# Optimization experiments

Measured on AMD Instinct MI355X. Metric: run time of the kernel, lower is better.

Reference implementation:

```python
import jax, jax.numpy as jnp
import numpy as np
from jax import lax

B, T, N = 4, 48, 2000
F, H, HEADS, HOR, K = 16, 64, 4, 24, 3
P = H // 2
EPS_BN = 1e-5
EPS_LN = 1e-5
NEG = -1e9


def layer_norm(x, g, b):
    mu = jnp.mean(x, axis=-1, keepdims=True)
    var = jnp.var(x, axis=-1, keepdims=True)
    return (x - mu) * jax.lax.rsqrt(var + EPS_LN) * g + b


def setup_inputs() -> dict:
    key = jax.random.key(0)
    ks = jax.random.split(key, 16)
    s = lambda k, shp, sc: jax.random.normal(k, shp, jnp.float32) * sc
    return {
        "x": s(ks[0], (B, T, N), 1.0),
        "conv_w": s(ks[1], (F, 1, K), 0.3),
        "conv_b": jnp.zeros((F,), jnp.float32),
        "bn_g": jnp.ones((F,), jnp.float32),
        "bn_b": jnp.zeros((F,), jnp.float32),
        "proj_w": s(ks[2], (H, F * T), 0.03),
        "proj_b": jnp.zeros((H,), jnp.float32),
        "ln1_g": jnp.ones((H,), jnp.float32),
        "ln1_b": jnp.zeros((H,), jnp.float32),
        "src_w": s(ks[3], (P, H), 0.1),
        "src_b": jnp.zeros((P,), jnp.float32),
        "dst_w": s(ks[4], (P, H), 0.1),
        "dst_b": jnp.zeros((P,), jnp.float32),
        "edge_scale": jnp.ones((1,), jnp.float32),
        "in_proj_w": s(ks[5], (3 * H, H), 0.1),
        "in_proj_b": jnp.zeros((3 * H,), jnp.float32),
        "out_w": s(ks[6], (H, H), 0.1),
        "out_b": jnp.zeros((H,), jnp.float32),
        "lnA_g": jnp.ones((H,), jnp.float32),
        "lnA_b": jnp.zeros((H,), jnp.float32),
        "pred_w": s(ks[7], (HOR, H), 0.1),
        "pred_b": jnp.zeros((HOR,), jnp.float32),
    }


def reference(x, conv_w, conv_b, bn_g, bn_b, proj_w, proj_b, ln1_g, ln1_b,
              src_w, src_b, dst_w, dst_b, edge_scale,
              in_proj_w, in_proj_b, out_w, out_b, lnA_g, lnA_b,
              pred_w, pred_b):
    # ---- temporal encoding: [B,T,N] -> [B*N,1,T] conv1d(same) ----
    xt = jnp.transpose(x, (0, 2, 1)).reshape(B * N, 1, T)
    h = lax.conv_general_dilated(xt, conv_w, (1,), "SAME",
                                 dimension_numbers=("NCH", "OIH", "NCH"))
    h = h + conv_b[None, :, None]
    # BatchNorm1d in eval mode (running_mean=0, running_var=1)
    h = h * (bn_g * lax.rsqrt(jnp.float32(1.0 + EPS_BN)))[None, :, None] + bn_b[None, :, None]
    h = jax.nn.relu(h)
    # ---- feature projector: flatten [F,T] -> hidden ----
    flat = h.reshape(B * N, F * T)
    z = flat @ proj_w.T + proj_b
    z = jax.nn.relu(layer_norm(z, ln1_g, ln1_b))
    node = z.reshape(B, N, H)
    # ---- dynamic graph generation ----
    src = jax.nn.leaky_relu(node @ src_w.T + src_b, 0.2)  # [B,N,P]
    dst = jax.nn.leaky_relu(node @ dst_w.T + dst_b, 0.2)
    adj = jnp.einsum("bnp,bmp->bnm", src, dst) * edge_scale[0]
    norm = jnp.maximum(jnp.linalg.norm(adj, axis=-1, keepdims=True), 1e-12)
    adj = adj / norm + jnp.eye(N, dtype=adj.dtype)[None]
    neg_mask = jnp.where(adj <= 0, jnp.float32(NEG), jnp.float32(0.0))  # [B,N,N]
    # ---- relational attention (single layer) ----
    residual = node
    qkv = node @ in_proj_w.T + in_proj_b  # [B,N,3H]
    q, k, v = jnp.split(qkv, 3, axis=-1)
    d = H // HEADS
    qh = q.reshape(B, N, HEADS, d)
    kh = k.reshape(B, N, HEADS, d)
    vh = v.reshape(B, N, HEADS, d)
    scores = jnp.einsum("bqhd,bkhd->bhqk", qh, kh) / jnp.sqrt(jnp.float32(d))
    attn = jax.nn.softmax(scores, axis=-1)
    y = jnp.einsum("bhqk,bkhd->bqhd", attn, vh).reshape(B, N, H)
    y = y @ out_w.T + out_b
    # second (adjacency-masked) attention recompute
    w2 = jnp.einsum("bnd,bmd->bnm", y, y) / jnp.sqrt(jnp.float32(H)) + neg_mask
    w2 = jax.nn.softmax(w2, axis=-1)
    y = jnp.einsum("bnm,bmd->bnd", w2, y)
    y = layer_norm(y + residual, lnA_g, lnA_b)
    # ---- horizon predictor ----
    return y @ pred_w.T + pred_b  # [B,N,HOR]
```

## Files before the change

kernel.cpp:

```cpp
#include <hip/hip_runtime.h>
#include <hip/hip_bf16.h>


#define NB 4
#define TT 48
#define NNODES 2000
#define HORZ 24

#define D4(a,b) ((a).x*(b).x + (a).y*(b).y + (a).z*(b).z + (a).w*(b).w)
#define FMA4(o,p,v) { (o).x = fmaf((p),(v).x,(o).x); (o).y = fmaf((p),(v).y,(o).y); \
                      (o).z = fmaf((p),(v).z,(o).z); (o).w = fmaf((p),(v).w,(o).w); }

__device__ __forceinline__ float wsum64(float v) {
#pragma unroll
    for (int m = 1; m < 64; m <<= 1) v += __shfl_xor(v, m, 64);
    return v;
}

__global__ __launch_bounds__(256) void k_tr(const float* __restrict__ pw,
                                            float* __restrict__ pT) {
    int i = blockIdx.x * 256 + threadIdx.x;
    int h = i / 768, j = i - h * 768;
    pT[((j >> 2) * 64 + h) * 4 + (j & 3)] = pw[i];
}

__global__ __launch_bounds__(64) void k_enc(const float* __restrict__ x,
        const float* __restrict__ cw, const float* __restrict__ cb,
        const float* __restrict__ bg, const float* __restrict__ bb,
        const float* __restrict__ pT, const float* __restrict__ pb,
        const float* __restrict__ g1, const float* __restrict__ b1,
        float* __restrict__ node) {
    __shared__ float xs[8][52];
    __shared__ float hs[8][768];
    __shared__ float wc[16][4];
    int tid = threadIdx.x;
    int g0 = blockIdx.x * 8;

    if (tid < 16) {
        float s = bg[tid] * rsqrtf(1.0f + 1e-5f);
        wc[tid][0] = cw[tid * 3 + 0] * s;
        wc[tid][1] = cw[tid * 3 + 1] * s;
        wc[tid][2] = cw[tid * 3 + 2] * s;
        wc[tid][3] = cb[tid] * s + bb[tid];
    }
    for (int i = tid; i < 8 * TT; i += 64) {
        int m = i & 7, t = i >> 3;
        int g = g0 + m;
        int b = g / NNODES, n = g - b * NNODES;
        xs[m][t + 1] = x[(b * TT + t) * NNODES + n];
    }
    if (tid < 8) { xs[tid][0] = 0.f; xs[tid][TT + 1] = 0.f; }
    __syncthreads();

    for (int m = 0; m < 8; m++) {
        for (int j = tid; j < 16 * TT; j += 64) {
            int f = j / TT, t = j - f * TT;
            float h = wc[f][0] * xs[m][t] + wc[f][1] * xs[m][t + 1] +
                      wc[f][2] * xs[m][t + 2] + wc[f][3];
            hs[m][j] = fmaxf(h, 0.f);
        }
    }
    __syncthreads();

    float acc[8];
    float pbv = pb[tid];
#pragma unroll
    for (int m = 0; m < 8; m++) acc[m] = pbv;
    const float4* pT4v = (const float4*)pT;
    for (int jb = 0; jb < 192; ++jb) {
        float4 wv = pT4v[jb * 64 + tid];
#pragma unroll
        for (int m = 0; m < 8; m++) {
            float4 hv = *(const float4*)&hs[m][jb * 4];
            acc[m] += D4(wv, hv);
        }
    }
    float gg = g1[tid], bbv = b1[tid];
    for (int m = 0; m < 8; m++) {
        float v = acc[m];
        float sm = wsum64(v);
        float sq = wsum64(v * v);
        float mu = sm * (1.f / 64.f);
        float var = sq * (1.f / 64.f) - mu * mu;
        float z = (v - mu) * rsqrtf(var + 1e-5f) * gg + bbv;
        node[(g0 + m) * 64 + tid] = fmaxf(z, 0.f);
    }
}

__global__ __launch_bounds__(256) void k_qkv(const float* __restrict__ node,
        const float* __restrict__ ipw, const float* __restrict__ ipb,
        const float* __restrict__ sw, const float* __restrict__ sb,
        const float* __restrict__ dw, const float* __restrict__ db,
        float* __restrict__ Qb, float* __restrict__ Kb, float* __restrict__ Vb,
        float* __restrict__ Sb, float* __restrict__ Db) {
    __shared__ float nds[8][64];
    int tid = threadIdx.x;
    int g0 = blockIdx.x * 8;
    for (int i = tid; i < 8 * 64; i += 256) {
        nds[i >> 6][i & 63] = node[(size_t)g0 * 64 + i];
    }
    __syncthreads();

    int o = tid;
    const float* wrow; float bias;
    if (o < 192)      { wrow = ipw + o * 64;          bias = ipb[o]; }
    else if (o < 224) { wrow = sw + (o - 192) * 64;   bias = sb[o - 192]; }
    else              { wrow = dw + (o - 224) * 64;   bias = db[o - 224]; }

    float acc[8];
#pragma unroll
    for (int n = 0; n < 8; ++n) acc[n] = bias;

#pragma unroll
    for (int c = 0; c < 4; ++c) {
        const float4* wp = (const float4*)(wrow + c * 16);
        float4 w0 = wp[0], w1 = wp[1], w2 = wp[2], w3 = wp[3];
#pragma unroll
        for (int n = 0; n < 8; ++n) {
            const float4* nr = (const float4*)&nds[n][c * 16];
            float4 a0 = nr[0], a1 = nr[1], a2 = nr[2], a3 = nr[3];
            acc[n] += D4(a0, w0) + D4(a1, w1) + D4(a2, w2) + D4(a3, w3);
        }
    }

    if (o < 64) {
#pragma unroll
        for (int n = 0; n < 8; ++n) Qb[(size_t)(g0 + n) * 64 + o] = acc[n] * 0.25f;
    } else if (o < 128) {
        int oo = o - 64;
#pragma unroll
        for (int n = 0; n < 8; ++n) Kb[(size_t)(g0 + n) * 64 + oo] = acc[n];
    } else if (o < 192) {
        int oo = o - 128;
#pragma unroll
        for (int n = 0; n < 8; ++n) Vb[(size_t)(g0 + n) * 64 + oo] = acc[n];
    } else if (o < 224) {
        int oo = o - 192;
#pragma unroll
        for (int n = 0; n < 8; ++n) {
            float a = acc[n];
            Sb[(size_t)(g0 + n) * 32 + oo] = (a >= 0.f ? a : 0.2f * a);
        }
    } else {
        int oo = o - 224;
#pragma unroll
        for (int n = 0; n < 8; ++n) {
            float a = acc[n];
            Db[(size_t)(g0 + n) * 32 + oo] = (a >= 0.f ? a : 0.2f * a);
        }
    }
}

__global__ __launch_bounds__(256) void k_attn1p(const float* __restrict__ Qb,
        const float* __restrict__ Kb, const float* __restrict__ Vb,
        float* __restrict__ Part) {
    __shared__ float Kl[50 * 64];
    __shared__ float Vl[50 * 64];
    int tid = threadIdx.x, bid = blockIdx.x;
    int b = bid >> 7, rem = bid & 127, qt = rem >> 3, mc = rem & 7;
    int w = tid >> 6, l = tid & 63, h = l >> 4, qs = l & 15;
    size_t baseRow = (size_t)b * NNODES;
    int q0g = qt * 128 + w * 32 + qs * 2, q1g = q0g + 1;
    int q0i = min(q0g, NNODES - 1), q1i = min(q1g, NNODES - 1);

    const float4* qp0 = (const float4*)(Qb + (baseRow + q0i) * 64 + h * 16);
    float4 q0a = qp0[0], q0b = qp0[1], q0cc = qp0[2], q0d = qp0[3];
    const float4* qp1 = (const float4*)(Qb + (baseRow + q1i) * 64 + h * 16);
    float4 q1a = qp1[0], q1b = qp1[1], q1cc = qp1[2], q1d = qp1[3];

    float4 o0a = {0,0,0,0}, o0b = {0,0,0,0}, o0c = {0,0,0,0}, o0d = {0,0,0,0};
    float4 o1a = {0,0,0,0}, o1b = {0,0,0,0}, o1c = {0,0,0,0}, o1d = {0,0,0,0};
    float sum0 = 0.f, sum1 = 0.f;

    int m0 = mc * 250;
    for (int t = 0; t < 5; ++t) {
        int mb = m0 + t * 50;
        for (int i = tid; i < 1600; i += 256) {
            if (i < 800)
                ((float4*)Kl)[i] = *(const float4*)(Kb + (baseRow + mb + (i >> 4)) * 64 + (i & 15) * 4);
            else {
                int j = i - 800;
                ((float4*)Vl)[j] = *(const float4*)(Vb + (baseRow + mb + (j >> 4)) * 64 + (j & 15) * 4);
            }
        }
        __syncthreads();
        for (int mi = 0; mi < 50; ++mi) {
            const float4* K4 = (const float4*)(Kl + mi * 64 + h * 16);
            float4 k0 = K4[0], k1 = K4[1], k2 = K4[2], k3 = K4[3];
            float s0 = D4(q0a,k0) + D4(q0b,k1) + D4(q0cc,k2) + D4(q0d,k3);
            float s1 = D4(q1a,k0) + D4(q1b,k1) + D4(q1cc,k2) + D4(q1d,k3);
            float p0 = __expf(s0), p1 = __expf(s1);
            sum0 += p0; sum1 += p1;
            const float4* V4 = (const float4*)(Vl + mi * 64 + h * 16);
            float4 v0 = V4[0], v1 = V4[1], v2 = V4[2], v3 = V4[3];
            FMA4(o0a,p0,v0) FMA4(o0b,p0,v1) FMA4(o0c,p0,v2) FMA4(o0d,p0,v3)
            FMA4(o1a,p1,v0) FMA4(o1b,p1,v1) FMA4(o1c,p1,v2) FMA4(o1d,p1,v3)
        }
        __syncthreads();
    }
    if (q0g < NNODES) {
        size_t base = ((baseRow + q0g) * 8 + mc) * 68;
        float4* dst = (float4*)(Part + base + h * 16);
        dst[0] = o0a; dst[1] = o0b; dst[2] = o0c; dst[3] = o0d;
        Part[base + 64 + h] = sum0;
    }
    if (q1g < NNODES) {
        size_t base = ((baseRow + q1g) * 8 + mc) * 68;
        float4* dst = (float4*)(Part + base + h * 16);
        dst[0] = o1a; dst[1] = o1b; dst[2] = o1c; dst[3] = o1d;
        Part[base + 64 + h] = sum1;
    }
}

__global__ __launch_bounds__(256) void k_attn1m(const float* __restrict__ Part,
        const float* __restrict__ ow, const float* __restrict__ ob,
        float* __restrict__ y1) {
    __shared__ float ys[4][68];
    int tid = threadIdx.x, w = tid >> 6, l = tid & 63;
    int qg = blockIdx.x * 4 + w;
    int h = l >> 4, d = l & 15;
    float o = 0.f, sum = 0.f;
    size_t base = (size_t)qg * 8 * 68;
#pragma unroll
    for (int mc = 0; mc < 8; ++mc) {
        o   += Part[base + mc * 68 + h * 16 + d];
        sum += Part[base + mc * 68 + 64 + h];
    }
    ys[w][h * 16 + d] = o / sum;
    __syncthreads();
    float acc = ob[l];
    const float4* wr = (const float4*)(ow + l * 64);
#pragma unroll
    for (int e = 0; e < 16; ++e) {
        float4 yv = *(const float4*)&ys[w][e * 4];
        acc += D4(yv, wr[e]);
    }
    y1[(size_t)qg * 64 + l] = acc;
}

__global__ __launch_bounds__(256) void k_attn2p(const float* __restrict__ y1,
        const float* __restrict__ Sbuf, const float* __restrict__ Dbuf,
        const float* __restrict__ es_p, float* __restrict__ Part) {
    __shared__ float Yl[50 * 64];
    __shared__ float Dl[50 * 32];
    int tid = threadIdx.x, bid = blockIdx.x;
    int b = bid >> 7, rem = bid & 127, qt = rem >> 3, mc = rem & 7;
    int w = tid >> 6, l = tid & 63, c = l >> 4, qs = l & 15;
    size_t baseRow = (size_t)b * NNODES;
    float es = es_p[0];
    int q0g = qt * 128 + w * 32 + qs * 2, q1g = q0g + 1;
    int q0i = min(q0g, NNODES - 1), q1i = min(q1g, NNODES - 1);

    const float4* yp0 = (const float4*)(y1 + (baseRow + q0i) * 64 + c * 16);
    float4 yq0a = yp0[0], yq0b = yp0[1], yq0c = yp0[2], yq0d = yp0[3];
    const float4* yp1 = (const float4*)(y1 + (baseRow + q1i) * 64 + c * 16);
    float4 yq1a = yp1[0], yq1b = yp1[1], yq1c = yp1[2], yq1d = yp1[3];
    const float4* sp0 = (const float4*)(Sbuf + (baseRow + q0i) * 32 + c * 8);
    float4 sr0a = sp0[0], sr0b = sp0[1];
    const float4* sp1 = (const float4*)(Sbuf + (baseRow + q1i) * 32 + c * 8);
    float4 sr1a = sp1[0], sr1b = sp1[1];

    float4 o0a = {0,0,0,0}, o0b = {0,0,0,0}, o0c = {0,0,0,0}, o0d = {0,0,0,0};
    float4 o1a = {0,0,0,0}, o1b = {0,0,0,0}, o1c = {0,0,0,0}, o1d = {0,0,0,0};
    float sum0 = 0.f, sum1 = 0.f, ssq0 = 0.f, ssq1 = 0.f;
    float ad0 = 0.f, sd0 = 0.f, ad1 = 0.f, sd1 = 0.f;

    int m0 = mc * 250;
    for (int t = 0; t < 5; ++t) {
        int mb = m0 + t * 50;
        for (int i = tid; i < 1200; i += 256) {
            if (i < 800)
                ((float4*)Yl)[i] = *(const float4*)(y1 + (baseRow + mb + (i >> 4)) * 64 + (i & 15) * 4);
            else {
                int j = i - 800;
                ((float4*)Dl)[j] = *(const float4*)(Dbuf + (baseRow + mb + (j >> 3)) * 32 + (j & 7) * 4);
            }
        }
        __syncthreads();
        for (int mi = 0; mi < 50; ++mi) {
            int mg = mb + mi;
            const float4* Y4 = (const float4*)(Yl + mi * 64 + c * 16);
            float4 ya = Y4[0], yb = Y4[1], yc = Y4[2], yd = Y4[3];
            const float4* Dd = (const float4*)(Dl + mi * 32 + c * 8);
            float4 da = Dd[0], db2 = Dd[1];
            float s0 = D4(yq0a,ya) + D4(yq0b,yb) + D4(yq0c,yc) + D4(yq0d,yd);
            float s1 = D4(yq1a,ya) + D4(yq1b,yb) + D4(yq1c,yc) + D4(yq1d,yd);
            float a0 = D4(sr0a,da) + D4(sr0b,db2);
            float a1 = D4(sr1a,da) + D4(sr1b,db2);
            s0 += __shfl_xor(s0, 16, 64); s0 += __shfl_xor(s0, 32, 64);
            s1 += __shfl_xor(s1, 16, 64); s1 += __shfl_xor(s1, 32, 64);
            a0 += __shfl_xor(a0, 16, 64); a0 += __shfl_xor(a0, 32, 64);
            a1 += __shfl_xor(a1, 16, 64); a1 += __shfl_xor(a1, 32, 64);
            a0 *= es; a1 *= es;
            ssq0 += a0 * a0; ssq1 += a1 * a1;
            float p0 = (a0 > 0.f) ? __expf(s0 * 0.125f) : 0.f;
            float p1 = (a1 > 0.f) ? __expf(s1 * 0.125f) : 0.f;
            if (mg == q0g) { ad0 = a0; sd0 = s0; p0 = 0.f; }
            if (mg == q1g) { ad1 = a1; sd1 = s1; p1 = 0.f; }
            sum0 += p0; sum1 += p1;
            FMA4(o0a,p0,ya) FMA4(o0b,p0,yb) FMA4(o0c,p0,yc) FMA4(o0d,p0,yd)
            FMA4(o1a,p1,ya) FMA4(o1b,p1,yb) FMA4(o1c,p1,yc) FMA4(o1d,p1,yd)
        }
        __syncthreads();
    }
    if (q0g < NNODES) {
        size_t base = ((baseRow + q0g) * 8 + mc) * 68;
        float4* dst = (float4*)(Part + base + c * 16);
        dst[0] = o0a; dst[1] = o0b; dst[2] = o0c; dst[3] = o0d;
        if (c == 0) *(float4*)(Part + base + 64) = make_float4(sum0, ssq0, ad0, sd0);
    }
    if (q1g < NNODES) {
        size_t base = ((baseRow + q1g) * 8 + mc) * 68;
        float4* dst = (float4*)(Part + base + c * 16);
        dst[0] = o1a; dst[1] = o1b; dst[2] = o1c; dst[3] = o1d;
        if (c == 0) *(float4*)(Part + base + 64) = make_float4(sum1, ssq1, ad1, sd1);
    }
}

__global__ __launch_bounds__(256) void k_attn2m(const float* __restrict__ Part,
        const float* __restrict__ y1, const float* __restrict__ node,
        const float* __restrict__ ga, const float* __restrict__ ba,
        const float* __restrict__ pw, const float* __restrict__ pb,
        float* __restrict__ out) {
    __shared__ float zs[4][68];
    int tid = threadIdx.x, w = tid >> 6, l = tid & 63;
    int qg = blockIdx.x * 4 + w;
    float o = 0.f, sum = 0.f, ssq = 0.f, ad = 0.f, sd = 0.f;
    size_t base = (size_t)qg * 8 * 68;
#pragma unroll
    for (int mc = 0; mc < 8; ++mc) {
        o += Part[base + mc * 68 + l];
        float4 sc = *(const float4*)(Part + base + mc * 68 + 64);
        sum += sc.x; ssq += sc.y; ad += sc.z; sd += sc.w;
    }
    float norm = fmaxf(sqrtf(ssq), 1e-12f);
    float yv = y1[(size_t)qg * 64 + l];
    if (ad > -norm) {
        float pd = __expf(sd * 0.125f);
        sum += pd;
        o = fmaf(pd, yv, o);
    }
    float oo = o / sum + node[(size_t)qg * 64 + l];
    float s1 = wsum64(oo), s2 = wsum64(oo * oo);
    float mu = s1 * (1.f / 64.f);
    float var = s2 * (1.f / 64.f) - mu * mu;
    float rs = rsqrtf(var + 1e-5f);
    zs[w][l] = (oo - mu) * rs * ga[l] + ba[l];
    __syncthreads();
    if (l < HORZ) {
        float acc = pb[l];
        const float4* pr = (const float4*)(pw + l * 64);
#pragma unroll
        for (int e = 0; e < 16; ++e) {
            float4 zv = *(const float4*)&zs[w][e * 4];
            acc += D4(zv, pr[e]);
        }
        out[(size_t)qg * HORZ + l] = acc;
    }
}

extern "C" void kernel_launch(void* const* d_in, const int* in_sizes, int n_in,
                              void* d_out, int out_size, void* d_ws, size_t ws_size,
                              hipStream_t stream) {
    const float* x      = (const float*)d_in[0];
    const float* conv_w = (const float*)d_in[1];
    const float* conv_b = (const float*)d_in[2];
    const float* bn_g   = (const float*)d_in[3];
    const float* bn_b   = (const float*)d_in[4];
    const float* proj_w = (const float*)d_in[5];
    const float* proj_b = (const float*)d_in[6];
    const float* ln1_g  = (const float*)d_in[7];
    const float* ln1_b  = (const float*)d_in[8];
    const float* src_w  = (const float*)d_in[9];
    const float* src_b  = (const float*)d_in[10];
    const float* dst_w  = (const float*)d_in[11];
    const float* dst_b  = (const float*)d_in[12];
    const float* edge_s = (const float*)d_in[13];
    const float* ipw    = (const float*)d_in[14];
    const float* ipb    = (const float*)d_in[15];
    const float* out_w  = (const float*)d_in[16];
    const float* out_b  = (const float*)d_in[17];
    const float* lnA_g  = (const float*)d_in[18];
    const float* lnA_b  = (const float*)d_in[19];
    const float* pred_w = (const float*)d_in[20];
    const float* pred_b = (const float*)d_in[21];
    float* out = (float*)d_out;

    float* ws    = (float*)d_ws;
    float* projT = ws;
    float* node  = projT + 49152;
    float* y1    = node + 512000;
    float* Qb    = y1 + 512000;
    float* Kb    = Qb + 512000;
    float* Vb    = Kb + 512000;
    float* Sbuf  = Vb + 512000;
    float* Dbuf  = Sbuf + 256000;
    float* Part  = Dbuf + 256000;

    k_tr<<<192, 256, 0, stream>>>(proj_w, projT);
    k_enc<<<8000 / 8, 64, 0, stream>>>(x, conv_w, conv_b, bn_g, bn_b,
                                       projT, proj_b, ln1_g, ln1_b, node);
    k_qkv<<<8000 / 8, 256, 0, stream>>>(node, ipw, ipb, src_w, src_b, dst_w, dst_b,
                                        Qb, Kb, Vb, Sbuf, Dbuf);
    k_attn1p<<<512, 256, 0, stream>>>(Qb, Kb, Vb, Part);
    k_attn1m<<<2000, 256, 0, stream>>>(Part, out_w, out_b, y1);
    k_attn2p<<<512, 256, 0, stream>>>(y1, Sbuf, Dbuf, edge_s, Part);
    k_attn2m<<<2000, 256, 0, stream>>>(Part, y1, node, lnA_g, lnA_b,
                                       pred_w, pred_b, out);
}
```

Before: 436.3 us.

## Precompute adjacency as bitmask and restructure attention to one query per thread

```diff
diff --git a/kernel.cpp b/kernel.cpp
--- a/kernel.cpp
+++ b/kernel.cpp
@@ -6,6 +6,7 @@
 #define TT 48
 #define NNODES 2000
 #define HORZ 24
+#define PART_Q 8000
 
 #define D4(a,b) ((a).x*(b).x + (a).y*(b).y + (a).z*(b).z + (a).w*(b).w)
 #define FMA4(o,p,v) { (o).x = fmaf((p),(v).x,(o).x); (o).y = fmaf((p),(v).y,(o).y); \
@@ -151,211 +152,314 @@
     }
 }
 
-__global__ __launch_bounds__(256) void k_attn1p(const float* __restrict__ Qb,
+__global__ __launch_bounds__(256) void k_adj(const float* __restrict__ Sbuf,
+        const float* __restrict__ Dbuf, const float* __restrict__ es_p,
+        unsigned* __restrict__ maskU, float* __restrict__ ssqP,
+        float* __restrict__ adv) {
+    __shared__ float Sl[64][32];
+    __shared__ float ssqW[4][64];
+    int tid = threadIdx.x, bid = blockIdx.x;
+    int b = bid >> 7, qt = (bid >> 2) & 31, mc = bid & 3;
+    int w = tid >> 6, l = tid & 63;
+    int bbase = b * NNODES;
+    int qg0 = bbase + qt * 64;
+    float es = es_p[0];
+
+    for (int k = 0; k < 2; ++k) {
+        int idx = tid + k * 256;
+        int row = idx >> 3, cc = idx & 7;
+        int qv = qt * 64 + row;
+        *(float4*)&Sl[row][cc * 4] =
+            *(const float4*)(Sbuf + (size_t)(bbase + min(qv, NNODES - 1)) * 32 + cc * 4);
+    }
+    __syncthreads();
+
+    float ssqAcc = 0.f;
+#pragma unroll
+    for (int tt = 0; tt < 2; ++tt) {
+        int t = w + tt * 4;
+        int mtb = mc * 512 + t * 64;
+        int mb = mtb + l;
+        bool mok = mb < NNODES;
+        float4 dr[8];
+        const float4* dp = (const float4*)(Dbuf + (size_t)(bbase + (mok ? mb : NNODES - 1)) * 32);
+#pragma unroll
+        for (int j = 0; j < 8; ++j) dr[j] = dp[j];
+
+        unsigned lo = 0, hi = 0;
+        for (int qq = 0; qq < 64; ++qq) {
+            int qv = qt * 64 + qq;
+            const float4* sp = (const float4*)&Sl[qq][0];
+            float a = 0.f;
+#pragma unroll
+            for (int j = 0; j < 8; ++j) a += D4(sp[j], dr[j]);
+            a *= es;
+            if (!mok) a = 0.f;
+            bool diag = (mb == qv);
+            if (diag && qv < NNODES) adv[qg0 + qq - bbase + bbase] = a;
+            bool bit = (a > 0.f) && !diag;
+            float ssqq = wsum64(a * a);
+            unsigned long long bal = __ballot(bit);
+            if (qq == l) { lo = (unsigned)bal; hi = (unsigned)(bal >> 32); ssqAcc += ssqq; }
+        }
+        int qv = qt * 64 + l;
+        if (qv < NNODES) {
+            int widx = mc * 16 + t * 2;
+            maskU[(size_t)widx * PART_Q + qg0 + l] = lo;
+            maskU[(size_t)(widx + 1) * PART_Q + qg0 + l] = hi;
+        }
+    }
+    ssqW[w][l] = ssqAcc;
+    __syncthreads();
+    if (tid < 64) {
+        int qv = qt * 64 + tid;
+        if (qv < NNODES)
+            ssqP[(size_t)mc * PART_Q + qg0 + tid] =
+                ssqW[0][tid] + ssqW[1][tid] + ssqW[2][tid] + ssqW[3][tid];
+    }
+}
+
+__global__ __launch_bounds__(256) void k_diag(const float* __restrict__ ssqP,
+        const float* __restrict__ adv, unsigned* __restrict__ maskU) {
+    int qg = blockIdx.x * 256 + threadIdx.x;
+    if (qg >= PART_Q) return;
+    float ss = ssqP[qg] + ssqP[PART_Q + qg] + ssqP[2 * PART_Q + qg] + ssqP[3 * PART_Q + qg];
+    float norm = fmaxf(sqrtf(ss), 1e-12f);
+    float ad = adv[qg];
+    if (ad > -norm) {
+        int qloc = qg % NNODES;
+        size_t idx = (size_t)(qloc >> 5) * PART_Q + qg;
+        maskU[idx] |= (1u << (qloc & 31));
+    }
+}
+
+__global__ __launch_bounds__(256, 2) void k_a1(const float* __restrict__ Qb,
         const float* __restrict__ Kb, const float* __restrict__ Vb,
         float* __restrict__ Part) {
-    __shared__ float Kl[50 * 64];
-    __shared__ float Vl[50 * 64];
+    __shared__ float Kl[125][64];
+    __shared__ float Vl[125][64];
     int tid = threadIdx.x, bid = blockIdx.x;
-    int b = bid >> 7, rem = bid & 127, qt = rem >> 3, mc = rem & 7;
-    int w = tid >> 6, l = tid & 63, h = l >> 4, qs = l & 15;
-    size_t baseRow = (size_t)b * NNODES;
-    int q0g = qt * 128 + w * 32 + qs * 2, q1g = q0g + 1;
-    int q0i = min(q0g, NNODES - 1), q1i = min(q1g, NNODES - 1);
-
-    const float4* qp0 = (const float4*)(Qb + (baseRow + q0i) * 64 + h * 16);
-    float4 q0a = qp0[0], q0b = qp0[1], q0cc = qp0[2], q0d = qp0[3];
-    const float4* qp1 = (const float4*)(Qb + (baseRow + q1i) * 64 + h * 16);
-    float4 q1a = qp1[0], q1b = qp1[1], q1cc = qp1[2], q1d = qp1[3];
-
-    float4 o0a = {0,0,0,0}, o0b = {0,0,0,0}, o0c = {0,0,0,0}, o0d = {0,0,0,0};
-    float4 o1a = {0,0,0,0}, o1b = {0,0,0,0}, o1c = {0,0,0,0}, o1d = {0,0,0,0};
-    float sum0 = 0.f, sum1 = 0.f;
-
-    int m0 = mc * 250;
-    for (int t = 0; t < 5; ++t) {
-        int mb = m0 + t * 50;
-        for (int i = tid; i < 1600; i += 256) {
-            if (i < 800)
-                ((float4*)Kl)[i] = *(const float4*)(Kb + (baseRow + mb + (i >> 4)) * 64 + (i & 15) * 4);
-            else {
-                int j = i - 800;
-                ((float4*)Vl)[j] = *(const float4*)(Vb + (baseRow + mb + (j >> 4)) * 64 + (j & 15) * 4);
-            }
-        }
-        __syncthreads();
-        for (int mi = 0; mi < 50; ++mi) {
-            const float4* K4 = (const float4*)(Kl + mi * 64 + h * 16);
-            float4 k0 = K4[0], k1 = K4[1], k2 = K4[2], k3 = K4[3];
-            float s0 = D4(q0a,k0) + D4(q0b,k1) + D4(q0cc,k2) + D4(q0d,k3);
-            float s1 = D4(q1a,k0) + D4(q1b,k1) + D4(q1cc,k2) + D4(q1d,k3);
-            float p0 = __expf(s0), p1 = __expf(s1);
-            sum0 += p0; sum1 += p1;
-            const float4* V4 = (const float4*)(Vl + mi * 64 + h * 16);
-            float4 v0 = V4[0], v1 = V4[1], v2 = V4[2], v3 = V4[3];
-            FMA4(o0a,p0,v0) FMA4(o0b,p0,v1) FMA4(o0c,p0,v2) FMA4(o0d,p0,v3)
-            FMA4(o1a,p1,v0) FMA4(o1b,p1,v1) FMA4(o1c,p1,v2) FMA4(o1d,p1,v3)
-        }
-        __syncthreads();
-    }
-    if (q0g < NNODES) {
-        size_t base = ((baseRow + q0g) * 8 + mc) * 68;
-        float4* dst = (float4*)(Part + base + h * 16);
-        dst[0] = o0a; dst[1] = o0b; dst[2] = o0c; dst[3] = o0d;
-        Part[base + 64 + h] = sum0;
-    }
-    if (q1g < NNODES) {
-        size_t base = ((baseRow + q1g) * 8 + mc) * 68;
-        float4* dst = (float4*)(Part + base + h * 16);
-        dst[0] = o1a; dst[1] = o1b; dst[2] = o1c; dst[3] = o1d;
-        Part[base + 64 + h] = sum1;
-    }
-}
-
-__global__ __launch_bounds__(256) void k_attn1m(const float* __restrict__ Part,
+    int b = bid >> 7, qb = (bid >> 4) & 7, mc = bid & 15;
+    int bbase = b * NNODES;
+    int qloc = qb * 256 + tid;
+    int qg = bbase + qloc;
+    int qi = bbase + min(qloc, NNODES - 1);
+
+    for (int k = 0; k < 16; ++k) {
+        int idx = tid + k * 256;
+        if (idx < 4000) {
+            int arr = idx >= 2000 ? 1 : 0;
+            int e = arr ? idx - 2000 : idx;
+            int r = e >> 4, cc = e & 15;
+            int mb = mc * 125 + r;
+            float4 v = *(const float4*)((arr ? Vb : Kb) + (size_t)(bbase + mb) * 64 + cc * 4);
+            float* dst = arr ? &Vl[0][0] : &Kl[0][0];
+            *(float4*)(dst + r * 64 + cc * 4) = v;
+        }
+    }
+
+    float4 q[16];
+    const float4* qp = (const float4*)(Qb + (size_t)qi * 64);
+#pragma unroll
+    for (int j = 0; j < 16; ++j) q[j] = qp[j];
+    float4 fo[16];
+#pragma unroll
+    for (int j = 0; j < 16; ++j) fo[j] = make_float4(0.f, 0.f, 0.f, 0.f);
+    float sm[4] = {0.f, 0.f, 0.f, 0.f};
+    __syncthreads();
+
+    for (int mi = 0; mi < 125; ++mi) {
+        const float4* kr = (const float4*)&Kl[mi][0];
+        float p[4];
+#pragma unroll
+        for (int h = 0; h < 4; ++h) {
+            float4 k0 = kr[h * 4], k1 = kr[h * 4 + 1], k2 = kr[h * 4 + 2], k3 = kr[h * 4 + 3];
+            float s = D4(q[h * 4], k0) + D4(q[h * 4 + 1], k1) +
+                      D4(q[h * 4 + 2], k2) + D4(q[h * 4 + 3], k3);
+            p[h] = __expf(s);
+            sm[h] += p[h];
+        }
+        const float4* vr = (const float4*)&Vl[mi][0];
+#pragma unroll
+        for (int j = 0; j < 16; ++j) {
+            float4 v = vr[j];
+            FMA4(fo[j], p[j >> 2], v)
+        }
+    }
+
+    if (qloc < NNODES) {
+        float* base = Part + (size_t)(mc * 68) * PART_Q + qg;
+#pragma unroll
+        for (int j = 0; j < 16; ++j) {
+            base[(size_t)(4 * j + 0) * PART_Q] = fo[j].x;
+            base[(size_t)(4 * j + 1) * PART_Q] = fo[j].y;
+            base[(size_t)(4 * j + 2) * PART_Q] = fo[j].z;
+            base[(size_t)(4 * j + 3) * PART_Q] = fo[j].w;
+        }
+#pragma unroll
+        for (int h = 0; h < 4; ++h) base[(size_t)(64 + h) * PART_Q] = sm[h];
+    }
+}
+
+__global__ __launch_bounds__(256) void k_a1m(const float* __restrict__ Part,
         const float* __restrict__ ow, const float* __restrict__ ob,
         float* __restrict__ y1) {
-    __shared__ float ys[4][68];
-    int tid = threadIdx.x, w = tid >> 6, l = tid & 63;
-    int qg = blockIdx.x * 4 + w;
-    int h = l >> 4, d = l & 15;
-    float o = 0.f, sum = 0.f;
-    size_t base = (size_t)qg * 8 * 68;
-#pragma unroll
-    for (int mc = 0; mc < 8; ++mc) {
-        o   += Part[base + mc * 68 + h * 16 + d];
-        sum += Part[base + mc * 68 + 64 + h];
-    }
-    ys[w][h * 16 + d] = o / sum;
-    __syncthreads();
-    float acc = ob[l];
-    const float4* wr = (const float4*)(ow + l * 64);
-#pragma unroll
-    for (int e = 0; e < 16; ++e) {
-        float4 yv = *(const float4*)&ys[w][e * 4];
-        acc += D4(yv, wr[e]);
-    }
-    y1[(size_t)qg * 64 + l] = acc;
-}
-
-__global__ __launch_bounds__(256) void k_attn2p(const float* __restrict__ y1,
-        const float* __restrict__ Sbuf, const float* __restrict__ Dbuf,
-        const float* __restrict__ es_p, float* __restrict__ Part) {
-    __shared__ float Yl[50 * 64];
-    __shared__ float Dl[50 * 32];
+    __shared__ float owl[64][64];
+    int tid = threadIdx.x;
+    for (int i = tid; i < 4096; i += 256) ((float*)owl)[i] = ow[i];
+    __syncthreads();
+    int qg = blockIdx.x * 256 + tid;
+    if (qg >= PART_Q) return;
+    float acc[68];
+#pragma unroll
+    for (int k = 0; k < 68; ++k) acc[k] = 0.f;
+    for (int mc = 0; mc < 16; ++mc) {
+        const float* p = Part + (size_t)(mc * 68) * PART_Q + qg;
+#pragma unroll
+        for (int k = 0; k < 68; ++k) acc[k] += p[(size_t)k * PART_Q];
+    }
+#pragma unroll
+    for (int e = 0; e < 64; ++e) acc[e] /= acc[64 + (e >> 4)];
+    float* yo = y1 + (size_t)qg * 64;
+    for (int d = 0; d < 64; d += 4) {
+        float4 r;
+        float rr[4];
+#pragma unroll
+        for (int u = 0; u < 4; ++u) {
+            float s = ob[d + u];
+            const float4* wr = (const float4*)&owl[d + u][0];
+#pragma unroll
+            for (int e4 = 0; e4 < 16; ++e4) {
+                float4 w4 = wr[e4];
+                s = fmaf(acc[e4 * 4 + 0], w4.x, s);
+                s = fmaf(acc[e4 * 4 + 1], w4.y, s);
+                s = fmaf(acc[e4 * 4 + 2], w4.z, s);
+                s = fmaf(acc[e4 * 4 + 3], w4.w, s);
+            }
+            rr[u] = s;
+        }
+        r = make_float4(rr[0], rr[1], rr[2], rr[3]);
+        *(float4*)(yo + d) = r;
+    }
+}
+
+__global__ __launch_bounds__(256, 2) void k_a2(const float* __restrict__ y1,
+        const unsigned* __restrict__ maskU, float* __restrict__ Part) {
+    __shared__ float Yl[128][64];
     int tid = threadIdx.x, bid = blockIdx.x;
-    int b = bid >> 7, rem = bid & 127, qt = rem >> 3, mc = rem & 7;
-    int w = tid >> 6, l = tid & 63, c = l >> 4, qs = l & 15;
-    size_t baseRow = (size_t)b * NNODES;
-    float es = es_p[0];
-    int q0g = qt * 128 + w * 32 + qs * 2, q1g = q0g + 1;
-    int q0i = min(q0g, NNODES - 1), q1i = min(q1g, NNODES - 1);
-
-    const float4* yp0 = (const float4*)(y1 + (baseRow + q0i) * 64 + c * 16);
-    float4 yq0a = yp0[0], yq0b = yp0[1], yq0c = yp0[2], yq0d = yp0[3];
-    const float4* yp1 = (const float4*)(y1 + (baseRow + q1i) * 64 + c * 16);
-    float4 yq1a = yp1[0], yq1b = yp1[1], yq1c = yp1[2], yq1d = yp1[3];
-    const float4* sp0 = (const float4*)(Sbuf + (baseRow + q0i) * 32 + c * 8);
-    float4 sr0a = sp0[0], sr0b = sp0[1];
-    const float4* sp1 = (const float4*)(Sbuf + (baseRow + q1i) * 32 + c * 8);
-    float4 sr1a = sp1[0], sr1b = sp1[1];
-
-    float4 o0a = {0,0,0,0}, o0b = {0,0,0,0}, o0c = {0,0,0,0}, o0d = {0,0,0,0};
-    float4 o1a = {0,0,0,0}, o1b = {0,0,0,0}, o1c = {0,0,0,0}, o1d = {0,0,0,0};
-    float sum0 = 0.f, sum1 = 0.f, ssq0 = 0.f, ssq1 = 0.f;
-    float ad0 = 0.f, sd0 = 0.f, ad1 = 0.f, sd1 = 0.f;
-
-    int m0 = mc * 250;
-    for (int t = 0; t < 5; ++t) {
-        int mb = m0 + t * 50;
-        for (int i = tid; i < 1200; i += 256) {
-            if (i < 800)
-                ((float4*)Yl)[i] = *(const float4*)(y1 + (baseRow + mb + (i >> 4)) * 64 + (i & 15) * 4);
-            else {
-                int j = i - 800;
-                ((float4*)Dl)[j] = *(const float4*)(Dbuf + (baseRow + mb + (j >> 3)) * 32 + (j & 7) * 4);
-            }
-        }
-        __syncthreads();
-        for (int mi = 0; mi < 50; ++mi) {
-            int mg = mb + mi;
-            const float4* Y4 = (const float4*)(Yl + mi * 64 + c * 16);
-            float4 ya = Y4[0], yb = Y4[1], yc = Y4[2], yd = Y4[3];
-            const float4* Dd = (const float4*)(Dl + mi * 32 + c * 8);
-            float4 da = Dd[0], db2 = Dd[1];
-            float s0 = D4(yq0a,ya) + D4(yq0b,yb) + D4(yq0c,yc) + D4(yq0d,yd);
-            float s1 = D4(yq1a,ya) + D4(yq1b,yb) + D4(yq1c,yc) + D4(yq1d,yd);
-            float a0 = D4(sr0a,da) + D4(sr0b,db2);
-            float a1 = D4(sr1a,da) + D4(sr1b,db2);
-            s0 += __shfl_xor(s0, 16, 64); s0 += __shfl_xor(s0, 32, 64);
-            s1 += __shfl_xor(s1, 16, 64); s1 += __shfl_xor(s1, 32, 64);
-            a0 += __shfl_xor(a0, 16, 64); a0 += __shfl_xor(a0, 32, 64);
-            a1 += __shfl_xor(a1, 16, 64); a1 += __shfl_xor(a1, 32, 64);
-            a0 *= es; a1 *= es;
-            ssq0 += a0 * a0; ssq1 += a1 * a1;
-            float p0 = (a0 > 0.f) ? __expf(s0 * 0.125f) : 0.f;
-            float p1 = (a1 > 0.f) ? __expf(s1 * 0.125f) : 0.f;
-            if (mg == q0g) { ad0 = a0; sd0 = s0; p0 = 0.f; }
-            if (mg == q1g) { ad1 = a1; sd1 = s1; p1 = 0.f; }
-            sum0 += p0; sum1 += p1;
-            FMA4(o0a,p0,ya) FMA4(o0b,p0,yb) FMA4(o0c,p0,yc) FMA4(o0d,p0,yd)
-            FMA4(o1a,p1,ya) FMA4(o1b,p1,yb) FMA4(o1c,p1,yc) FMA4(o1d,p1,yd)
-        }
-        __syncthreads();
-    }
-    if (q0g < NNODES) {
-        size_t base = ((baseRow + q0g) * 8 + mc) * 68;
-        float4* dst = (float4*)(Part + base + c * 16);
-        dst[0] = o0a; dst[1] = o0b; dst[2] = o0c; dst[3] = o0d;
-        if (c == 0) *(float4*)(Part + base + 64) = make_float4(sum0, ssq0, ad0, sd0);
-    }
-    if (q1g < NNODES) {
-        size_t base = ((baseRow + q1g) * 8 + mc) * 68;
-        float4* dst = (float4*)(Part + base + c * 16);
-        dst[0] = o1a; dst[1] = o1b; dst[2] = o1c; dst[3] = o1d;
-        if (c == 0) *(float4*)(Part + base + 64) = make_float4(sum1, ssq1, ad1, sd1);
-    }
-}
-
-__global__ __launch_bounds__(256) void k_attn2m(const float* __restrict__ Part,
-        const float* __restrict__ y1, const float* __restrict__ node,
+    int b = bid >> 7, qb = (bid >> 4) & 7, mc = bid & 15;
+    int bbase = b * NNODES;
+    int qloc = qb * 256 + tid;
+    int qg = bbase + qloc;
+    int qgc = bbase + min(qloc, NNODES - 1);
+
+    for (int k = 0; k < 8; ++k) {
+        int idx = tid + k * 256;
+        int r = idx >> 4, cc = idx & 15;
+        int mb = mc * 128 + r;
+        float4 v = make_float4(0.f, 0.f, 0.f, 0.f);
+        if (mb < NNODES)
+            v = *(const float4*)(y1 + (size_t)(bbase + mb) * 64 + cc * 4);
+        *(float4*)&Yl[r][cc * 4] = v;
+    }
+
+    float4 yq[16];
+    const float4* qp = (const float4*)(y1 + (size_t)qgc * 64);
+#pragma unroll
+    for (int j = 0; j < 16; ++j) yq[j] = qp[j];
+    float4 o[16];
+#pragma unroll
+    for (int j = 0; j < 16; ++j) o[j] = make_float4(0.f, 0.f, 0.f, 0.f);
+    float sum = 0.f;
+    unsigned mw = 0;
+    __syncthreads();
+
+    for (int mi = 0; mi < 128; ++mi) {
+        if ((mi & 31) == 0) mw = maskU[(size_t)(mc * 4 + (mi >> 5)) * PART_Q + qgc];
+        const float4* yr4 = (const float4*)&Yl[mi][0];
+        float4 yr[16];
+#pragma unroll
+        for (int j = 0; j < 16; ++j) yr[j] = yr4[j];
+        float s0 = 0.f, s1 = 0.f, s2 = 0.f, s3 = 0.f;
+#pragma unroll
+        for (int j = 0; j < 4; ++j) {
+            s0 += D4(yq[j], yr[j]);
+            s1 += D4(yq[4 + j], yr[4 + j]);
+            s2 += D4(yq[8 + j], yr[8 + j]);
+            s3 += D4(yq[12 + j], yr[12 + j]);
+        }
+        float s = (s0 + s1) + (s2 + s3);
+        float p = ((mw >> (mi & 31)) & 1u) ? __expf(s * 0.125f) : 0.f;
+        sum += p;
+#pragma unroll
+        for (int j = 0; j < 16; ++j) FMA4(o[j], p, yr[j])
+    }
+
+    if (qloc < NNODES) {
+        float* base = Part + (size_t)(mc * 68) * PART_Q + qg;
+#pragma unroll
+        for (int j = 0; j < 16; ++j) {
+            base[(size_t)(4 * j + 0) * PART_Q] = o[j].x;
+            base[(size_t)(4 * j + 1) * PART_Q] = o[j].y;
+            base[(size_t)(4 * j + 2) * PART_Q] = o[j].z;
+            base[(size_t)(4 * j + 3) * PART_Q] = o[j].w;
+        }
+        base[(size_t)64 * PART_Q] = sum;
+    }
+}
+
+__global__ __launch_bounds__(256) void k_a2m(const float* __restrict__ Part,
+        const float* __restrict__ node,
         const float* __restrict__ ga, const float* __restrict__ ba,
         const float* __restrict__ pw, const float* __restrict__ pb,
         float* __restrict__ out) {
-    __shared__ float zs[4][68];
-    int tid = threadIdx.x, w = tid >> 6, l = tid & 63;
-    int qg = blockIdx.x * 4 + w;
-    float o = 0.f, sum = 0.f, ssq = 0.f, ad = 0.f, sd = 0.f;
-    size_t base = (size_t)qg * 8 * 68;
-#pragma unroll
-    for (int mc = 0; mc < 8; ++mc) {
-        o += Part[base + mc * 68 + l];
-        float4 sc = *(const float4*)(Part + base + mc * 68 + 64);
-        sum += sc.x; ssq += sc.y; ad += sc.z; sd += sc.w;
-    }
-    float norm = fmaxf(sqrtf(ssq), 1e-12f);
-    float yv = y1[(size_t)qg * 64 + l];
-    if (ad > -norm) {
-        float pd = __expf(sd * 0.125f);
-        sum += pd;
-        o = fmaf(pd, yv, o);
-    }
-    float oo = o / sum + node[(size_t)qg * 64 + l];
-    float s1 = wsum64(oo), s2 = wsum64(oo * oo);
+    __shared__ float pwl[24][64];
+    __shared__ float gal[64], bal[64], pbl[24];
+    int tid = threadIdx.x;
+    for (int i = tid; i < 24 * 64; i += 256) ((float*)pwl)[i] = pw[i];
+    if (tid < 64) { gal[tid] = ga[tid]; bal[tid] = ba[tid]; }
+    if (tid < 24) pbl[tid] = pb[tid];
+    __syncthreads();
+    int qg = blockIdx.x * 256 + tid;
+    if (qg >= PART_Q) return;
+
+    float acc[65];
+#pragma unroll
+    for (int k = 0; k < 65; ++k) acc[k] = 0.f;
+    for (int mc = 0; mc < 16; ++mc) {
+        const float* p = Part + (size_t)(mc * 68) * PART_Q + qg;
+#pragma unroll
+        for (int k = 0; k < 65; ++k) acc[k] += p[(size_t)k * PART_Q];
+    }
+    float inv = 1.0f / acc[64];
+    const float* nd = node + (size_t)qg * 64;
+    float oo[64];
+    float s1 = 0.f, s2 = 0.f;
+#pragma unroll
+    for (int d = 0; d < 64; ++d) {
+        float v = acc[d] * inv + nd[d];
+        oo[d] = v;
+        s1 += v; s2 += v * v;
+    }
     float mu = s1 * (1.f / 64.f);
     float var = s2 * (1.f / 64.f) - mu * mu;
     float rs = rsqrtf(var + 1e-5f);
-    zs[w][l] = (oo - mu) * rs * ga[l] + ba[l];
-    __syncthreads();
-    if (l < HORZ) {
-        float acc = pb[l];
-        const float4* pr = (const float4*)(pw + l * 64);
-#pragma unroll
-        for (int e = 0; e < 16; ++e) {
-            float4 zv = *(const float4*)&zs[w][e * 4];
-            acc += D4(zv, pr[e]);
-        }
-        out[(size_t)qg * HORZ + l] = acc;
+#pragma unroll
+    for (int d = 0; d < 64; ++d) oo[d] = (oo[d] - mu) * rs * gal[d] + bal[d];
+
+    float* op = out + (size_t)qg * HORZ;
+    for (int r = 0; r < HORZ; ++r) {
+        float s = pbl[r];
+        const float4* wr = (const float4*)&pwl[r][0];
+#pragma unroll
+        for (int e4 = 0; e4 < 16; ++e4) {
+            float4 w4 = wr[e4];
+            s = fmaf(oo[e4 * 4 + 0], w4.x, s);
+            s = fmaf(oo[e4 * 4 + 1], w4.y, s);
+            s = fmaf(oo[e4 * 4 + 2], w4.z, s);
+            s = fmaf(oo[e4 * 4 + 3], w4.w, s);
+        }
+        op[r] = s;
     }
 }
 
@@ -386,25 +490,29 @@
     const float* pred_b = (const float*)d_in[21];
     float* out = (float*)d_out;
 
-    float* ws    = (float*)d_ws;
-    float* projT = ws;
-    float* node  = projT + 49152;
-    float* y1    = node + 512000;
-    float* Qb    = y1 + 512000;
-    float* Kb    = Qb + 512000;
-    float* Vb    = Kb + 512000;
-    float* Sbuf  = Vb + 512000;
-    float* Dbuf  = Sbuf + 256000;
-    float* Part  = Dbuf + 256000;
+    float* ws = (float*)d_ws;
+    float*    projT = ws;
+    float*    node  = projT + 49152;
+    float*    y1    = node + 512000;
+    float*    Qb    = y1 + 512000;
+    float*    Kb    = Qb + 512000;
+    float*    Vb    = Kb + 512000;
+    float*    Sbuf  = Vb + 512000;
+    float*    Dbuf  = Sbuf + 256000;
+    unsigned* maskU = (unsigned*)(Dbuf + 256000);
+    float*    ssqP  = (float*)(maskU + 512000);
+    float*    adv   = ssqP + 32000;
+    float*    Part  = adv + 8000;
 
     k_tr<<<192, 256, 0, stream>>>(proj_w, projT);
-    k_enc<<<8000 / 8, 64, 0, stream>>>(x, conv_w, conv_b, bn_g, bn_b,
-                                       projT, proj_b, ln1_g, ln1_b, node);
-    k_qkv<<<8000 / 8, 256, 0, stream>>>(node, ipw, ipb, src_w, src_b, dst_w, dst_b,
-                                        Qb, Kb, Vb, Sbuf, Dbuf);
-    k_attn1p<<<512, 256, 0, stream>>>(Qb, Kb, Vb, Part);
-    k_attn1m<<<2000, 256, 0, stream>>>(Part, out_w, out_b, y1);
-    k_attn2p<<<512, 256, 0, stream>>>(y1, Sbuf, Dbuf, edge_s, Part);
-    k_attn2m<<<2000, 256, 0, stream>>>(Part, y1, node, lnA_g, lnA_b,
-                                       pred_w, pred_b, out);
-}
+    k_enc<<<1000, 64, 0, stream>>>(x, conv_w, conv_b, bn_g, bn_b,
+                                   projT, proj_b, ln1_g, ln1_b, node);
+    k_qkv<<<1000, 256, 0, stream>>>(node, ipw, ipb, src_w, src_b, dst_w, dst_b,
+                                    Qb, Kb, Vb, Sbuf, Dbuf);
+    k_adj<<<512, 256, 0, stream>>>(Sbuf, Dbuf, edge_s, maskU, ssqP, adv);
+    k_diag<<<32, 256, 0, stream>>>(ssqP, adv, maskU);
+    k_a1<<<512, 256, 0, stream>>>(Qb, Kb, Vb, Part);
+    k_a1m<<<32, 256, 0, stream>>>(Part, out_w, out_b, y1);
+    k_a2<<<512, 256, 0, stream>>>(y1, maskU, Part);
+    k_a2m<<<32, 256, 0, stream>>>(Part, node, lnA_g, lnA_b, pred_w, pred_b, out);
+}
```

Result: slower. 523.4 us (+20.0%).
